# Optimization experiments

Hardware: AMD Instinct MI355X
Metric: run time of the kernel (lower is better)

## Reference

```python
import jax, jax.numpy as jnp
import numpy as np

B, S, D, H = 2, 4096, 1024, 16
DK = D // H


def setup_inputs() -> dict:
    key = jax.random.key(0)
    ks = jax.random.split(key, 8)
    scale = 1.0 / np.sqrt(D)
    return {
        "q": jax.random.normal(ks[0], (B, S, D), dtype=jnp.float32),
        "k": jax.random.normal(ks[1], (B, S, D), dtype=jnp.float32),
        "v": jax.random.normal(ks[2], (B, S, D), dtype=jnp.float32),
        "mask": jax.random.randint(ks[3], (1, 1, S, S), 0, 2, dtype=jnp.int32),
        "w_q": jax.random.normal(ks[4], (D, D), dtype=jnp.float32) * scale,
        "w_k": jax.random.normal(ks[5], (D, D), dtype=jnp.float32) * scale,
        "w_v": jax.random.normal(ks[6], (D, D), dtype=jnp.float32) * scale,
        "w_o": jax.random.normal(ks[7], (D, D), dtype=jnp.float32) * scale,
    }


def reference(q, k, v, mask, w_q, w_k, w_v, w_o):
    # torch Linear(bias=False): y = x @ W.T
    def proj_split(x, w):
        y = jnp.einsum("bsd,ed->bse", x, w)  # [B,S,D]
        return y.reshape(x.shape[0], -1, H, DK).transpose(0, 2, 1, 3)  # [B,H,S,dk]

    Q = proj_split(q, w_q)
    K = proj_split(k, w_k)
    V = proj_split(v, w_v)

    scores = jnp.einsum("bhqd,bhkd->bhqk", Q, K) / jnp.sqrt(jnp.float32(DK))
    scores = jnp.where(mask == 0, jnp.float32(-1e9), scores)
    attn = jax.nn.softmax(scores, axis=-1)  # dropout p=0 -> identity
    ctx = jnp.einsum("bhqk,bhkd->bhqd", attn, V)  # [B,H,S,dk]
    ctx = ctx.transpose(0, 2, 1, 3).reshape(q.shape[0], -1, D)  # [B,S,D]
    return jnp.einsum("bsd,ed->bse", ctx, w_o)
```

## Files before the change

kernel.cpp:

```cpp
#include <hip/hip_runtime.h>
#include <math.h>
#include <stdint.h>

constexpr int B = 2, S = 4096, D = 1024, H = 16, DK = 64;
constexpr int M_TOT = B * S;

typedef __attribute__((ext_vector_type(8))) short bf16x8;
typedef __attribute__((ext_vector_type(4))) float f32x4;
typedef unsigned short u16;

__device__ inline u16 f2bf(float f) {
    uint32_t u = __builtin_bit_cast(uint32_t, f);
    u += 0x7fffu + ((u >> 16) & 1u);
    return (u16)(u >> 16);
}

__device__ inline u16 f2bf_hw(float f) {
    __bf16 h = (__bf16)f;
    return __builtin_bit_cast(u16, h);
}

__device__ inline void gl2lds16(const void* g, void* l) {
    __builtin_amdgcn_global_load_lds((const __attribute__((address_space(1))) void*)g,
                                     (__attribute__((address_space(3))) void*)l, 16, 0, 0);
}

__global__ __launch_bounds__(256) void conv_bf16(const float* __restrict__ s0, const float* __restrict__ s1,
                                                 const float* __restrict__ s2, const float* __restrict__ s3,
                                                 u16* __restrict__ d0, u16* __restrict__ d1,
                                                 u16* __restrict__ d2, u16* __restrict__ d3, int n) {
    const float* s; u16* d;
    switch (blockIdx.y) {
        case 0: s = s0; d = d0; break;
        case 1: s = s1; d = d1; break;
        case 2: s = s2; d = d2; break;
        default: s = s3; d = d3; break;
    }
    const int i = (blockIdx.x * 256 + threadIdx.x) * 4;
    if (i < n) {
        float4 v = *(const float4*)(s + i);
        ushort4 o;
        o.x = f2bf(v.x); o.y = f2bf(v.y); o.z = f2bf(v.z); o.w = f2bf(v.w);
        *(ushort4*)(d + i) = o;
    }
}

__global__ __launch_bounds__(256) void mask_pack(const int* __restrict__ m, uint32_t* __restrict__ out) {
    const int i = blockIdx.x * 256 + threadIdx.x;
    const int base = i * 32;
    uint32_t b = 0;
#pragma unroll
    for (int j = 0; j < 32; ++j) b |= (m[base + j] != 0 ? 1u : 0u) << j;
    out[i] = b;
}

template <typename OutT>
__global__ __launch_bounds__(256) void gemm_bt(const u16* __restrict__ X, const u16* __restrict__ Wm,
                                               OutT* __restrict__ Y, int M, int N, int K, float oscale) {
    __shared__ u16 As[128 * 64];
    __shared__ u16 Bs[128 * 64];
    const int tid = threadIdx.x;
    const int lane = tid & 63;
    const int wave = tid >> 6;
    const int l15 = lane & 15;
    const int quad = lane >> 4;
    const int i0 = blockIdx.x * 128;
    const int j0 = blockIdx.y * 128;
    const int wm = wave & 1, wn = wave >> 1;
    const int lr = lane >> 3;
    const int lc = (lane & 7) * 8;

    f32x4 zero = {0.f, 0.f, 0.f, 0.f};
    f32x4 acc[4][4];
#pragma unroll
    for (int a = 0; a < 4; ++a)
#pragma unroll
        for (int b2 = 0; b2 < 4; ++b2) acc[a][b2] = zero;

    for (int k0 = 0; k0 < K; k0 += 64) {
#pragma unroll
        for (int c = 0; c < 4; ++c) {
            const int ch = wave * 4 + c;
            const int row = ch * 8 + lr;
            gl2lds16(X + (size_t)(i0 + row) * K + k0 + lc, &As[ch * 512]);
            gl2lds16(Wm + (size_t)(j0 + row) * K + k0 + lc, &Bs[ch * 512]);
        }
        __syncthreads();
        bf16x8 af[4][2];
#pragma unroll
        for (int mt = 0; mt < 4; ++mt)
#pragma unroll
            for (int ks = 0; ks < 2; ++ks)
                af[mt][ks] = *(const bf16x8*)&As[(wm * 64 + mt * 16 + l15) * 64 + ks * 32 + quad * 8];
#pragma unroll
        for (int nt = 0; nt < 4; ++nt) {
#pragma unroll
            for (int ks = 0; ks < 2; ++ks) {
                bf16x8 bfr = *(const bf16x8*)&Bs[(wn * 64 + nt * 16 + l15) * 64 + ks * 32 + quad * 8];
#pragma unroll
                for (int mt = 0; mt < 4; ++mt)
                    acc[mt][nt] = __builtin_amdgcn_mfma_f32_16x16x32_bf16(af[mt][ks], bfr, acc[mt][nt], 0, 0, 0);
            }
        }
        __syncthreads();
    }
#pragma unroll
    for (int mt = 0; mt < 4; ++mt) {
#pragma unroll
        for (int r = 0; r < 4; ++r) {
            const int gi = i0 + wm * 64 + mt * 16 + quad * 4 + r;
#pragma unroll
            for (int nt = 0; nt < 4; ++nt) {
                const int gj = j0 + wn * 64 + nt * 16 + l15;
                const float v = acc[mt][nt][r] * oscale;
                if constexpr (sizeof(OutT) == 2) {
                    Y[(size_t)gi * N + gj] = (OutT)f2bf(v);
                } else {
                    Y[(size_t)gi * N + gj] = v;
                }
            }
        }
    }
}

__global__ __launch_bounds__(256) void attn_mfma(const u16* __restrict__ Qb, const u16* __restrict__ Kb,
                                                 const u16* __restrict__ Vt,
                                                 const uint64_t* __restrict__ mask64,
                                                 u16* __restrict__ ctx) {
    __shared__ u16 Ks[64 * 64];
    __shared__ u16 Vs[64 * 64];
    __shared__ u16 Ps[4][32 * 72];
    const int tid = threadIdx.x;
    const int lane = tid & 63;
    const int wave = tid >> 6;
    const int l15 = lane & 15;
    const int quad = lane >> 4;
    const int q0 = blockIdx.x * 128;
    const int bh = blockIdx.y;
    const int bb = bh >> 4, hh = bh & 15;
    const int mbase = bb * S;
    const int e0 = hh * DK;
    const int r7 = l15 & 7;

    const int srow = tid >> 2;
    const int scb = tid & 3;

    bf16x8 aq[2][2];
#pragma unroll
    for (int mi = 0; mi < 2; ++mi) {
        const u16* qrow = Qb + (size_t)(mbase + q0 + wave * 32 + mi * 16 + l15) * D + e0;
        aq[mi][0] = *(const bf16x8*)(qrow);
        aq[mi][0] = *(const bf16x8*)(qrow + quad * 8);
        aq[mi][1] = *(const bf16x8*)(qrow + 32 + quad * 8);
    }

    f32x4 O[2][4];
    f32x4 Ol[2];
#pragma unroll
    for (int mi = 0; mi < 2; ++mi) {
        Ol[mi] = (f32x4){0.f, 0.f, 0.f, 0.f};
#pragma unroll
        for (int dt = 0; dt < 4; ++dt) O[mi][dt] = (f32x4){0.f, 0.f, 0.f, 0.f};
    }

    bf16x8 ONES;
#pragma unroll
    for (int i = 0; i < 8; ++i) ONES[i] = (short)0x3F80;

    const uint64_t* mrow[2];
#pragma unroll
    for (int mi = 0; mi < 2; ++mi)
        mrow[mi] = mask64 + (size_t)(q0 + wave * 32 + mi * 16 + quad * 4) * (S / 64);

    for (int kt = 0; kt < S / 64; ++kt) {
        const int kb = kt * 64;
#pragma unroll
        for (int it = 0; it < 2; ++it) {
            const int cb = scb + it * 4;
            const int phys = cb ^ (srow & 7);
            const bf16x8 kvv = *(const bf16x8*)(Kb + (size_t)(mbase + kb + srow) * D + e0 + cb * 8);
            const bf16x8 vvv = *(const bf16x8*)(Vt + (size_t)(e0 + srow) * M_TOT + mbase + kb + cb * 8);
            *(bf16x8*)&Ks[srow * 64 + phys * 8] = kvv;
            *(bf16x8*)&Vs[srow * 64 + phys * 8] = vvv;
        }
        __syncthreads();

        bf16x8 kf[4][2];
#pragma unroll
        for (int nt = 0; nt < 4; ++nt) {
            kf[nt][0] = *(const bf16x8*)&Ks[(nt * 16 + l15) * 64 + (quad ^ r7) * 8];
            kf[nt][1] = *(const bf16x8*)&Ks[(nt * 16 + l15) * 64 + ((quad + 4) ^ r7) * 8];
        }

#pragma unroll
        for (int mi = 0; mi < 2; ++mi) {
            f32x4 sa[4];
#pragma unroll
            for (int nt = 0; nt < 4; ++nt) {
                f32x4 c = {0.f, 0.f, 0.f, 0.f};
                c = __builtin_amdgcn_mfma_f32_16x16x32_bf16(aq[mi][0], kf[nt][0], c, 0, 0, 0);
                c = __builtin_amdgcn_mfma_f32_16x16x32_bf16(aq[mi][1], kf[nt][1], c, 0, 0, 0);
                sa[nt] = c;
            }
            uint32_t mlo[4], mhi[4];
#pragma unroll
            for (int r = 0; r < 4; ++r) {
                const uint64_t sh = mrow[mi][(size_t)r * (S / 64) + kt] >> l15;
                mlo[r] = (uint32_t)sh;
                mhi[r] = (uint32_t)(sh >> 32);
            }
            u16* pw = &Ps[wave][mi * 16 * 72];
#pragma unroll
            for (int nt = 0; nt < 4; ++nt) {
#pragma unroll
                for (int r = 0; r < 4; ++r) {
                    const uint32_t w32 = (nt < 2) ? mlo[r] : mhi[r];
                    const uint32_t bit = (w32 >> ((nt & 1) * 16)) & 1u;
                    float p = __builtin_amdgcn_exp2f(sa[nt][r]);
                    p = bit ? p : 0.f;
                    pw[(quad * 4 + r) * 72 + nt * 16 + l15] = f2bf_hw(p);
                }
            }
        }

        bf16x8 ap[2][2];
#pragma unroll
        for (int mi = 0; mi < 2; ++mi)
#pragma unroll
            for (int ks = 0; ks < 2; ++ks)
                ap[mi][ks] = *(const bf16x8*)&Ps[wave][(mi * 16 + l15) * 72 + ks * 32 + quad * 8];

#pragma unroll
        for (int mi = 0; mi < 2; ++mi) {
            Ol[mi] = __builtin_amdgcn_mfma_f32_16x16x32_bf16(ap[mi][0], ONES, Ol[mi], 0, 0, 0);
            Ol[mi] = __builtin_amdgcn_mfma_f32_16x16x32_bf16(ap[mi][1], ONES, Ol[mi], 0, 0, 0);
        }
#pragma unroll
        for (int dt = 0; dt < 4; ++dt) {
            const bf16x8 bv0 = *(const bf16x8*)&Vs[(dt * 16 + l15) * 64 + (quad ^ r7) * 8];
            const bf16x8 bv1 = *(const bf16x8*)&Vs[(dt * 16 + l15) * 64 + ((quad + 4) ^ r7) * 8];
#pragma unroll
            for (int mi = 0; mi < 2; ++mi) {
                O[mi][dt] = __builtin_amdgcn_mfma_f32_16x16x32_bf16(ap[mi][0], bv0, O[mi][dt], 0, 0, 0);
                O[mi][dt] = __builtin_amdgcn_mfma_f32_16x16x32_bf16(ap[mi][1], bv1, O[mi][dt], 0, 0, 0);
            }
        }
        __syncthreads();
    }

#pragma unroll
    for (int mi = 0; mi < 2; ++mi) {
#pragma unroll
        for (int r = 0; r < 4; ++r) {
            const float inv = 1.f / Ol[mi][r];
            const int gm = mbase + q0 + wave * 32 + mi * 16 + quad * 4 + r;
#pragma unroll
            for (int dt = 0; dt < 4; ++dt)
                ctx[(size_t)gm * D + e0 + dt * 16 + l15] = f2bf(O[mi][dt][r] * inv);
        }
    }
}

extern "C" void kernel_launch(void* const* d_in, const int* in_sizes, int n_in,
                              void* d_out, int out_size, void* d_ws, size_t ws_size,
                              hipStream_t stream) {
    (void)in_sizes; (void)n_in; (void)out_size; (void)ws_size;
    const float* q = (const float*)d_in[0];
    const float* k = (const float*)d_in[1];
    const float* v = (const float*)d_in[2];
    const int* msk = (const int*)d_in[3];
    const float* w_q = (const float*)d_in[4];
    const float* w_k = (const float*)d_in[5];
    const float* w_v = (const float*)d_in[6];
    const float* w_o = (const float*)d_in[7];
    float* out = (float*)d_out;

    const size_t MB = 1u << 20;
    char* w = (char*)d_ws;
    u16* qb   = (u16*)(w + 0 * MB);
    u16* kb   = (u16*)(w + 16 * MB);
    u16* vb   = (u16*)(w + 32 * MB);
    u16* wqb  = (u16*)(w + 48 * MB);
    u16* wkb  = (u16*)(w + 50 * MB);
    u16* wvb  = (u16*)(w + 52 * MB);
    u16* wob  = (u16*)(w + 54 * MB);
    uint64_t* maskb = (uint64_t*)(w + 56 * MB);
    u16* Qf   = (u16*)(w + 58 * MB);
    u16* Kf   = (u16*)(w + 74 * MB);
    u16* Vtf  = (u16*)(w + 90 * MB);
    u16* ctxb = (u16*)(w + 106 * MB);

    const float SCL2 = 0.18033688011112042f;

    dim3 blk(256);
    conv_bf16<<<dim3(8192, 3), blk, 0, stream>>>(q, k, v, q, qb, kb, vb, qb, M_TOT * D);
    conv_bf16<<<dim3(1024, 4), blk, 0, stream>>>(w_q, w_k, w_v, w_o, wqb, wkb, wvb, wob, D * D);
    mask_pack<<<dim3(S * S / 32 / 256), blk, 0, stream>>>(msk, (uint32_t*)maskb);

    gemm_bt<u16><<<dim3(M_TOT / 128, D / 128), blk, 0, stream>>>(qb, wqb, Qf, M_TOT, D, D, SCL2);
    gemm_bt<u16><<<dim3(M_TOT / 128, D / 128), blk, 0, stream>>>(kb, wkb, Kf, M_TOT, D, D, 1.0f);
    gemm_bt<u16><<<dim3(D / 128, M_TOT / 128), blk, 0, stream>>>(wvb, vb, Vtf, D, M_TOT, D, 1.0f);

    attn_mfma<<<dim3(S / 128, B * H), blk, 0, stream>>>(Qf, Kf, Vtf, maskb, ctxb);

    gemm_bt<float><<<dim3(M_TOT / 128, D / 128), blk, 0, stream>>>(ctxb, wob, out, M_TOT, D, D, 1.0f);
}
```

Baseline: 598.8 us.

## Merge QKV projections into one launch and enlarge attention query tile with prefetch

Merges the three projection GEMMs into a single kernel launch, using blockIdx.y to pick the operands. The attention kernel now handles 256 query rows per block (64 per wave), so each K/V tile loaded into shared memory is reused across twice as many queries. The next K/V tile is prefetched into registers while the current one is computed, and all V fragments are hoisted out of the inner loop. The cost is higher register pressure and half as many attention blocks (512), which may hurt occupancy and load balance.

```diff
diff --git a/kernel.cpp b/kernel.cpp
--- a/kernel.cpp
+++ b/kernel.cpp
@@ -55,27 +55,23 @@
 }
 
 template <typename OutT>
-__global__ __launch_bounds__(256) void gemm_bt(const u16* __restrict__ X, const u16* __restrict__ Wm,
-                                               OutT* __restrict__ Y, int M, int N, int K, float oscale) {
-    __shared__ u16 As[128 * 64];
-    __shared__ u16 Bs[128 * 64];
+__device__ inline void gemm_core(const u16* __restrict__ X, const u16* __restrict__ Wm,
+                                 OutT* __restrict__ Y, int i0, int j0, int N, int K,
+                                 float oscale, u16* As, u16* Bs) {
     const int tid = threadIdx.x;
     const int lane = tid & 63;
     const int wave = tid >> 6;
     const int l15 = lane & 15;
     const int quad = lane >> 4;
-    const int i0 = blockIdx.x * 128;
-    const int j0 = blockIdx.y * 128;
     const int wm = wave & 1, wn = wave >> 1;
     const int lr = lane >> 3;
     const int lc = (lane & 7) * 8;
 
-    f32x4 zero = {0.f, 0.f, 0.f, 0.f};
     f32x4 acc[4][4];
 #pragma unroll
     for (int a = 0; a < 4; ++a)
 #pragma unroll
-        for (int b2 = 0; b2 < 4; ++b2) acc[a][b2] = zero;
+        for (int b2 = 0; b2 < 4; ++b2) acc[a][b2] = (f32x4){0.f, 0.f, 0.f, 0.f};
 
     for (int k0 = 0; k0 < K; k0 += 64) {
 #pragma unroll
@@ -123,19 +119,48 @@
     }
 }
 
+__global__ __launch_bounds__(256) void proj3(const u16* __restrict__ X0, const u16* __restrict__ X1,
+                                             const u16* __restrict__ X2, const u16* __restrict__ W0,
+                                             const u16* __restrict__ W1, const u16* __restrict__ W2,
+                                             u16* __restrict__ Y0, u16* __restrict__ Y1,
+                                             u16* __restrict__ Y2, float s0) {
+    __shared__ u16 As[128 * 64];
+    __shared__ u16 Bs[128 * 64];
+    const int z = blockIdx.y;
+    const u16 *X, *W;
+    u16* Y;
+    float osc = 1.0f;
+    if (z == 0) { X = X0; W = W0; Y = Y0; osc = s0; }
+    else if (z == 1) { X = X1; W = W1; Y = Y1; }
+    else { X = X2; W = W2; Y = Y2; }
+    const int MB_ = (z == 2) ? 8 : 64;
+    const int N = (z == 2) ? M_TOT : D;
+    const int bx = blockIdx.x;
+    const int i0 = (bx % MB_) * 128;
+    const int j0 = (bx / MB_) * 128;
+    gemm_core<u16>(X, W, Y, i0, j0, N, D, osc, As, Bs);
+}
+
+__global__ __launch_bounds__(256) void gemm_out(const u16* __restrict__ X, const u16* __restrict__ Wm,
+                                                float* __restrict__ Y) {
+    __shared__ u16 As[128 * 64];
+    __shared__ u16 Bs[128 * 64];
+    gemm_core<float>(X, Wm, Y, blockIdx.x * 128, blockIdx.y * 128, D, D, 1.0f, As, Bs);
+}
+
 __global__ __launch_bounds__(256) void attn_mfma(const u16* __restrict__ Qb, const u16* __restrict__ Kb,
                                                  const u16* __restrict__ Vt,
                                                  const uint64_t* __restrict__ mask64,
                                                  u16* __restrict__ ctx) {
     __shared__ u16 Ks[64 * 64];
     __shared__ u16 Vs[64 * 64];
-    __shared__ u16 Ps[4][32 * 72];
+    __shared__ u16 Ps[4][64 * 68];
     const int tid = threadIdx.x;
     const int lane = tid & 63;
     const int wave = tid >> 6;
     const int l15 = lane & 15;
     const int quad = lane >> 4;
-    const int q0 = blockIdx.x * 128;
+    const int q0 = blockIdx.x * 256;
     const int bh = blockIdx.y;
     const int bb = bh >> 4, hh = bh & 15;
     const int mbase = bb * S;
@@ -145,19 +170,18 @@
     const int srow = tid >> 2;
     const int scb = tid & 3;
 
-    bf16x8 aq[2][2];
-#pragma unroll
-    for (int mi = 0; mi < 2; ++mi) {
-        const u16* qrow = Qb + (size_t)(mbase + q0 + wave * 32 + mi * 16 + l15) * D + e0;
-        aq[mi][0] = *(const bf16x8*)(qrow);
+    bf16x8 aq[4][2];
+#pragma unroll
+    for (int mi = 0; mi < 4; ++mi) {
+        const u16* qrow = Qb + (size_t)(mbase + q0 + wave * 64 + mi * 16 + l15) * D + e0;
         aq[mi][0] = *(const bf16x8*)(qrow + quad * 8);
         aq[mi][1] = *(const bf16x8*)(qrow + 32 + quad * 8);
     }
 
-    f32x4 O[2][4];
-    f32x4 Ol[2];
-#pragma unroll
-    for (int mi = 0; mi < 2; ++mi) {
+    f32x4 O[4][4];
+    f32x4 Ol[4];
+#pragma unroll
+    for (int mi = 0; mi < 4; ++mi) {
         Ol[mi] = (f32x4){0.f, 0.f, 0.f, 0.f};
 #pragma unroll
         for (int dt = 0; dt < 4; ++dt) O[mi][dt] = (f32x4){0.f, 0.f, 0.f, 0.f};
@@ -167,23 +191,39 @@
 #pragma unroll
     for (int i = 0; i < 8; ++i) ONES[i] = (short)0x3F80;
 
-    const uint64_t* mrow[2];
-#pragma unroll
-    for (int mi = 0; mi < 2; ++mi)
-        mrow[mi] = mask64 + (size_t)(q0 + wave * 32 + mi * 16 + quad * 4) * (S / 64);
-
-    for (int kt = 0; kt < S / 64; ++kt) {
-        const int kb = kt * 64;
+    const uint64_t* mrow[4];
+#pragma unroll
+    for (int mi = 0; mi < 4; ++mi)
+        mrow[mi] = mask64 + (size_t)(q0 + wave * 64 + mi * 16 + quad * 4) * (S / 64);
+
+    bf16x8 kreg[2], vreg[2];
+#pragma unroll
+    for (int it = 0; it < 2; ++it) {
+        const int cb = scb + it * 4;
+        kreg[it] = *(const bf16x8*)(Kb + (size_t)(mbase + srow) * D + e0 + cb * 8);
+        vreg[it] = *(const bf16x8*)(Vt + (size_t)(e0 + srow) * M_TOT + mbase + cb * 8);
+    }
+
+    constexpr int NT = S / 64;
+    for (int kt = 0; kt < NT; ++kt) {
 #pragma unroll
         for (int it = 0; it < 2; ++it) {
             const int cb = scb + it * 4;
             const int phys = cb ^ (srow & 7);
-            const bf16x8 kvv = *(const bf16x8*)(Kb + (size_t)(mbase + kb + srow) * D + e0 + cb * 8);
-            const bf16x8 vvv = *(const bf16x8*)(Vt + (size_t)(e0 + srow) * M_TOT + mbase + kb + cb * 8);
-            *(bf16x8*)&Ks[srow * 64 + phys * 8] = kvv;
-            *(bf16x8*)&Vs[srow * 64 + phys * 8] = vvv;
+            *(bf16x8*)&Ks[srow * 64 + phys * 8] = kreg[it];
+            *(bf16x8*)&Vs[srow * 64 + phys * 8] = vreg[it];
         }
         __syncthreads();
+
+        if (kt + 1 < NT) {
+            const int kb = (kt + 1) * 64;
+#pragma unroll
+            for (int it = 0; it < 2; ++it) {
+                const int cb = scb + it * 4;
+                kreg[it] = *(const bf16x8*)(Kb + (size_t)(mbase + kb + srow) * D + e0 + cb * 8);
+                vreg[it] = *(const bf16x8*)(Vt + (size_t)(e0 + srow) * M_TOT + mbase + kb + cb * 8);
+            }
+        }
 
         bf16x8 kf[4][2];
 #pragma unroll
@@ -192,8 +232,9 @@
             kf[nt][1] = *(const bf16x8*)&Ks[(nt * 16 + l15) * 64 + ((quad + 4) ^ r7) * 8];
         }
 
-#pragma unroll
-        for (int mi = 0; mi < 2; ++mi) {
+        u16* pw = &Ps[wave][0];
+#pragma unroll
+        for (int mi = 0; mi < 4; ++mi) {
             f32x4 sa[4];
 #pragma unroll
             for (int nt = 0; nt < 4; ++nt) {
@@ -209,7 +250,6 @@
                 mlo[r] = (uint32_t)sh;
                 mhi[r] = (uint32_t)(sh >> 32);
             }
-            u16* pw = &Ps[wave][mi * 16 * 72];
 #pragma unroll
             for (int nt = 0; nt < 4; ++nt) {
 #pragma unroll
@@ -218,42 +258,39 @@
                     const uint32_t bit = (w32 >> ((nt & 1) * 16)) & 1u;
                     float p = __builtin_amdgcn_exp2f(sa[nt][r]);
                     p = bit ? p : 0.f;
-                    pw[(quad * 4 + r) * 72 + nt * 16 + l15] = f2bf_hw(p);
+                    pw[(mi * 16 + quad * 4 + r) * 68 + nt * 16 + l15] = f2bf_hw(p);
                 }
             }
         }
 
-        bf16x8 ap[2][2];
-#pragma unroll
-        for (int mi = 0; mi < 2; ++mi)
-#pragma unroll
-            for (int ks = 0; ks < 2; ++ks)
-                ap[mi][ks] = *(const bf16x8*)&Ps[wave][(mi * 16 + l15) * 72 + ks * 32 + quad * 8];
-
-#pragma unroll
-        for (int mi = 0; mi < 2; ++mi) {
-            Ol[mi] = __builtin_amdgcn_mfma_f32_16x16x32_bf16(ap[mi][0], ONES, Ol[mi], 0, 0, 0);
-            Ol[mi] = __builtin_amdgcn_mfma_f32_16x16x32_bf16(ap[mi][1], ONES, Ol[mi], 0, 0, 0);
-        }
+        bf16x8 bv[4][2];
 #pragma unroll
         for (int dt = 0; dt < 4; ++dt) {
-            const bf16x8 bv0 = *(const bf16x8*)&Vs[(dt * 16 + l15) * 64 + (quad ^ r7) * 8];
-            const bf16x8 bv1 = *(const bf16x8*)&Vs[(dt * 16 + l15) * 64 + ((quad + 4) ^ r7) * 8];
-#pragma unroll
-            for (int mi = 0; mi < 2; ++mi) {
-                O[mi][dt] = __builtin_amdgcn_mfma_f32_16x16x32_bf16(ap[mi][0], bv0, O[mi][dt], 0, 0, 0);
-                O[mi][dt] = __builtin_amdgcn_mfma_f32_16x16x32_bf16(ap[mi][1], bv1, O[mi][dt], 0, 0, 0);
+            bv[dt][0] = *(const bf16x8*)&Vs[(dt * 16 + l15) * 64 + (quad ^ r7) * 8];
+            bv[dt][1] = *(const bf16x8*)&Vs[(dt * 16 + l15) * 64 + ((quad + 4) ^ r7) * 8];
+        }
+
+#pragma unroll
+        for (int mi = 0; mi < 4; ++mi) {
+            const bf16x8 ap0 = *(const bf16x8*)&pw[(mi * 16 + l15) * 68 + quad * 8];
+            const bf16x8 ap1 = *(const bf16x8*)&pw[(mi * 16 + l15) * 68 + 32 + quad * 8];
+            Ol[mi] = __builtin_amdgcn_mfma_f32_16x16x32_bf16(ap0, ONES, Ol[mi], 0, 0, 0);
+            Ol[mi] = __builtin_amdgcn_mfma_f32_16x16x32_bf16(ap1, ONES, Ol[mi], 0, 0, 0);
+#pragma unroll
+            for (int dt = 0; dt < 4; ++dt) {
+                O[mi][dt] = __builtin_amdgcn_mfma_f32_16x16x32_bf16(ap0, bv[dt][0], O[mi][dt], 0, 0, 0);
+                O[mi][dt] = __builtin_amdgcn_mfma_f32_16x16x32_bf16(ap1, bv[dt][1], O[mi][dt], 0, 0, 0);
             }
         }
         __syncthreads();
     }
 
 #pragma unroll
-    for (int mi = 0; mi < 2; ++mi) {
+    for (int mi = 0; mi < 4; ++mi) {
 #pragma unroll
         for (int r = 0; r < 4; ++r) {
             const float inv = 1.f / Ol[mi][r];
-            const int gm = mbase + q0 + wave * 32 + mi * 16 + quad * 4 + r;
+            const int gm = mbase + q0 + wave * 64 + mi * 16 + quad * 4 + r;
 #pragma unroll
             for (int dt = 0; dt < 4; ++dt)
                 ctx[(size_t)gm * D + e0 + dt * 16 + l15] = f2bf(O[mi][dt][r] * inv);
@@ -297,11 +334,9 @@
     conv_bf16<<<dim3(1024, 4), blk, 0, stream>>>(w_q, w_k, w_v, w_o, wqb, wkb, wvb, wob, D * D);
     mask_pack<<<dim3(S * S / 32 / 256), blk, 0, stream>>>(msk, (uint32_t*)maskb);
 
-    gemm_bt<u16><<<dim3(M_TOT / 128, D / 128), blk, 0, stream>>>(qb, wqb, Qf, M_TOT, D, D, SCL2);
-    gemm_bt<u16><<<dim3(M_TOT / 128, D / 128), blk, 0, stream>>>(kb, wkb, Kf, M_TOT, D, D, 1.0f);
-    gemm_bt<u16><<<dim3(D / 128, M_TOT / 128), blk, 0, stream>>>(wvb, vb, Vtf, D, M_TOT, D, 1.0f);
-
-    attn_mfma<<<dim3(S / 128, B * H), blk, 0, stream>>>(Qf, Kf, Vtf, maskb, ctxb);
-
-    gemm_bt<float><<<dim3(M_TOT / 128, D / 128), blk, 0, stream>>>(ctxb, wob, out, M_TOT, D, D, 1.0f);
-}
+    proj3<<<dim3(512, 3), blk, 0, stream>>>(qb, kb, wvb, wqb, wkb, vb, Qf, Kf, Vtf, SCL2);
+
+    attn_mfma<<<dim3(S / 256, B * H), blk, 0, stream>>>(Qf, Kf, Vtf, maskb, ctxb);
+
+    gemm_out<<<dim3(M_TOT / 128, D / 128), blk, 0, stream>>>(ctxb, wob, out);
+}
```

Result: slower. 612.8 us (+2.4%).
